# Kernel optimization log

Measured on AMD Instinct MI355X. Metric: run time of the kernel, lower is better.

Reference implementation:

```python
import jax, jax.numpy as jnp
import numpy as np

N_NODES = 100000
N_EDGES = 200000  # per relation
D_NODE = 128
D_EDGE = 16
N_REL = 3  # agent-agent, agent-object, object-object


def setup_inputs() -> dict:
    key = jax.random.key(0)
    ks = jax.random.split(key, 6)
    x = jax.random.normal(ks[0], (N_NODES, D_NODE), dtype=jnp.float32)
    edge_attr = jax.random.normal(ks[1], (N_REL, N_EDGES, D_EDGE), dtype=jnp.float32)
    W_rel = jax.random.normal(ks[2], (N_REL, D_NODE, D_NODE), dtype=jnp.float32) / np.sqrt(D_NODE)
    We_rel = jax.random.normal(ks[3], (N_REL, D_EDGE, D_NODE), dtype=jnp.float32) / np.sqrt(D_EDGE)
    W_self = jax.random.normal(ks[4], (D_NODE, D_NODE), dtype=jnp.float32) / np.sqrt(D_NODE)
    b = jnp.zeros((D_NODE,), dtype=jnp.float32)
    edge_index = jax.random.randint(ks[5], (N_REL, N_EDGES, 2), 0, N_NODES, dtype=jnp.int32)
    return {"x": x, "edge_attr": edge_attr, "W_rel": W_rel, "We_rel": We_rel,
            "W_self": W_self, "b": b, "edge_index": edge_index}


def reference(x, edge_attr, W_rel, We_rel, W_self, b, edge_index):
    # Heterogeneous message passing: per relation r,
    #   msg_e = x[src_e] @ W_r + edge_attr_e @ We_r
    #   agg_r = scatter_add(msg, dst)
    # node update: relu(x @ W_self + sum_r agg_r + b)
    n = x.shape[0]
    src = edge_index[:, :, 0]  # [R, E]
    dst = edge_index[:, :, 1]  # [R, E]
    # gather source features per relation: [R, E, F]
    msgs = jnp.einsum('ref,rfo->reo', x[src], W_rel) \
         + jnp.einsum('reg,rgo->reo', edge_attr, We_rel)
    # scatter-add to destination nodes per relation -> [R, N, F]
    agg = jax.vmap(lambda m, d: jax.ops.segment_sum(m, d, num_segments=n))(msgs, dst)
    return jax.nn.relu(x @ W_self + agg.sum(axis=0) + b)
```

## Files before the change

kernel.cpp:

```cpp
#include <hip/hip_runtime.h>

#define NN 100000
#define NE 200000
#define DN 128
#define DE 16
#define NR 3
#define NEDGE (NR * NE)
#define NB1 98
#define NSTRIP 6250
#define GEMM_GRID 1024

typedef __attribute__((ext_vector_type(8))) short short8;
typedef __attribute__((ext_vector_type(4))) float f32x4;

__device__ __forceinline__ unsigned short f2bf(float f) {
    unsigned int u = __float_as_uint(f);
    u = (u + 0x7fffu + ((u >> 16) & 1u)) >> 16;
    return (unsigned short)u;
}

__global__ __launch_bounds__(256) void prep_kernel(
    const float* __restrict__ W_self, const float* __restrict__ W_rel,
    const float* __restrict__ We,
    unsigned short* __restrict__ Wt, unsigned short* __restrict__ Wea,
    const int* __restrict__ ei, unsigned* __restrict__ cur,
    unsigned char* __restrict__ tmp)
{
    const int id = blockIdx.x * 256 + threadIdx.x;
    if (id < 65536) {
        const int m = id >> 14, rem = id & 16383;
        const int k = rem >> 7, n = rem & 127;
        const float* src = (m == 0) ? W_self : (W_rel + (size_t)(m - 1) * 16384);
        Wt[m * 16384 + n * 128 + k] = f2bf(src[k * 128 + n]);
    } else if (id < 65536 + 8192) {
        const int wid = id - 65536;
        const int n = wid >> 6, k = wid & 63;
        const float v = (k < 48) ? We[(k >> 4) * 2048 + (k & 15) * 128 + n] : 0.f;
        Wea[n * 64 + k] = f2bf(v);
    }
    const int2* ei2 = (const int2*)ei;
    for (int eid = id; eid < NEDGE; eid += 262144) {
        const int2 e = ei2[eid];
        const unsigned pos = atomicAdd(&cur[e.y], 1u);
        tmp[eid] = (unsigned char)pos;
    }
}

__global__ __launch_bounds__(256, 2) void gemm_kernel(
    const float* __restrict__ x,
    const unsigned short* __restrict__ Wt,
    unsigned short* __restrict__ zb,
    unsigned short* __restrict__ y)
{
    const int tid = threadIdx.x;
    const int m = tid >> 6;
    const int lane = tid & 63;
    const int lm = lane & 15;
    const int lq = lane >> 4;

    short8 bfr[8][4];
    {
        const unsigned short* wp = Wt + (size_t)m * 16384;
        #pragma unroll
        for (int cg = 0; cg < 8; ++cg)
            #pragma unroll
            for (int ks = 0; ks < 4; ++ks)
                bfr[cg][ks] = *(const short8*)(wp + (cg * 16 + lm) * 128 + ks * 32 + lq * 8);
    }
    unsigned short* outp = (m == 0) ? zb : (y + (size_t)(m - 1) * NN * 128);

    int s = blockIdx.x;
    float4 xb[8];
    {
        const float* xp = x + (size_t)(s * 16 + lm) * 128 + lq * 8;
        #pragma unroll
        for (int ks = 0; ks < 4; ++ks) {
            xb[2 * ks]     = *(const float4*)(xp + ks * 32);
            xb[2 * ks + 1] = *(const float4*)(xp + ks * 32 + 4);
        }
    }

    while (true) {
        short8 af[4];
        #pragma unroll
        for (int ks = 0; ks < 4; ++ks) {
            short8 t;
            t[0] = f2bf(xb[2 * ks].x);     t[1] = f2bf(xb[2 * ks].y);
            t[2] = f2bf(xb[2 * ks].z);     t[3] = f2bf(xb[2 * ks].w);
            t[4] = f2bf(xb[2 * ks + 1].x); t[5] = f2bf(xb[2 * ks + 1].y);
            t[6] = f2bf(xb[2 * ks + 1].z); t[7] = f2bf(xb[2 * ks + 1].w);
            af[ks] = t;
        }
        const int sn = s + GEMM_GRID;
        if (sn < NSTRIP) {
            const float* xp = x + (size_t)(sn * 16 + lm) * 128 + lq * 8;
            #pragma unroll
            for (int ks = 0; ks < 4; ++ks) {
                xb[2 * ks]     = *(const float4*)(xp + ks * 32);
                xb[2 * ks + 1] = *(const float4*)(xp + ks * 32 + 4);
            }
        }
        f32x4 acc[8];
        #pragma unroll
        for (int cg = 0; cg < 8; ++cg) acc[cg] = (f32x4){0.f, 0.f, 0.f, 0.f};
        #pragma unroll
        for (int cg = 0; cg < 8; ++cg)
            #pragma unroll
            for (int ks = 0; ks < 4; ++ks)
                acc[cg] = __builtin_amdgcn_mfma_f32_16x16x32_bf16(bfr[cg][ks], af[ks], acc[cg], 0, 0, 0);
        unsigned short* rp = outp + (size_t)(s * 16 + lm) * 128 + lq * 4;
        #pragma unroll
        for (int cg = 0; cg < 8; ++cg) {
            ushort4 o;
            o.x = f2bf(acc[cg][0]); o.y = f2bf(acc[cg][1]);
            o.z = f2bf(acc[cg][2]); o.w = f2bf(acc[cg][3]);
            *(ushort4*)(rp + cg * 16) = o;
        }
        if (sn >= NSTRIP) break;
        s = sn;
    }
}

__global__ __launch_bounds__(256) void scan1_kernel(
    const unsigned* __restrict__ cnt, unsigned* __restrict__ offs,
    unsigned* __restrict__ bsum)
{
    __shared__ unsigned wtot[4];
    const int tid = threadIdx.x, lane = tid & 63, wv = tid >> 6;
    const int base = blockIdx.x * 1024 + tid * 4;
    unsigned c[4];
    #pragma unroll
    for (int j = 0; j < 4; ++j) c[j] = (base + j < NN) ? cnt[base + j] : 0u;
    const unsigned ts = c[0] + c[1] + c[2] + c[3];
    unsigned incl = ts;
    #pragma unroll
    for (int d = 1; d < 64; d <<= 1) {
        unsigned v = __shfl_up(incl, d, 64);
        if (lane >= d) incl += v;
    }
    if (lane == 63) wtot[wv] = incl;
    __syncthreads();
    unsigned woff = 0;
    for (int p = 0; p < 4; ++p) if (p < wv) woff += wtot[p];
    unsigned run = woff + incl - ts;
    #pragma unroll
    for (int j = 0; j < 4; ++j) {
        if (base + j < NN) offs[base + j] = run;
        run += c[j];
    }
    if (tid == 255) bsum[blockIdx.x] = woff + incl;
}

__global__ void scan2_kernel(unsigned* __restrict__ bsum)
{
    const int lane = threadIdx.x;
    unsigned v[2], s = 0;
    const int base = lane * 2;
    #pragma unroll
    for (int j = 0; j < 2; ++j) {
        v[j] = (base + j < NB1) ? bsum[base + j] : 0u;
        s += v[j];
    }
    unsigned incl = s;
    #pragma unroll
    for (int d = 1; d < 64; d <<= 1) {
        unsigned t = __shfl_up(incl, d, 64);
        if (lane >= d) incl += t;
    }
    unsigned run = incl - s;
    #pragma unroll
    for (int j = 0; j < 2; ++j) {
        if (base + j < NB1) bsum[base + j] = run;
        run += v[j];
    }
}

__global__ __launch_bounds__(256) void scan3_kernel(
    unsigned* __restrict__ offs, const unsigned* __restrict__ bsum)
{
    const int base = blockIdx.x * 1024 + threadIdx.x * 4;
    const unsigned add = bsum[blockIdx.x];
    #pragma unroll
    for (int j = 0; j < 4; ++j)
        if (base + j < NN) offs[base + j] += add;
    if (blockIdx.x == 0 && threadIdx.x == 0) offs[NN] = NEDGE;
}

__global__ __launch_bounds__(256) void fill_kernel(
    const int* __restrict__ ei, const unsigned* __restrict__ offs,
    const unsigned char* __restrict__ tmp,
    unsigned* __restrict__ erow, unsigned* __restrict__ eeid)
{
    const int eid = blockIdx.x * 256 + threadIdx.x;
    if (eid < NEDGE) {
        const int2 e = ((const int2*)ei)[eid];
        const unsigned r = (eid >= 2 * NE) ? 2u : (eid >= NE ? 1u : 0u);
        const unsigned pos = offs[e.y] + (unsigned)tmp[eid];
        erow[pos] = r * NN + (unsigned)e.x;
        eeid[pos] = (unsigned)eid;
    }
}

__global__ __launch_bounds__(256, 4) void eaz_kernel(
    const float* __restrict__ edge_attr,
    const unsigned short* __restrict__ Wea,
    const unsigned* __restrict__ offs,
    const unsigned* __restrict__ eeid,
    unsigned short* __restrict__ zb)
{
    __shared__ __align__(16) unsigned short eaS[16][64];
    const int tid = threadIdx.x;
    const int wv = tid >> 6, lane = tid & 63;
    const int g = lane >> 4;
    const int k16 = lane & 15;
    const int row0 = blockIdx.x * 16;

    #pragma unroll
    for (int d = 0; d < 4; ++d) {
        const int dst = row0 + wv * 4 + d;
        const unsigned s = __builtin_amdgcn_readfirstlane(offs[dst]);
        const unsigned e = __builtin_amdgcn_readfirstlane(offs[dst + 1]);
        float ea = 0.f;
        unsigned py[8];
        #pragma unroll
        for (int j = 0; j < 8; ++j) {
            const unsigned q = eeid[s + j];
            py[j] = (q < (unsigned)NEDGE) ? q : 0u;
        }
        float a[8];
        #pragma unroll
        for (int j = 0; j < 8; ++j)
            a[j] = edge_attr[(size_t)py[j] * 16 + k16];
        #pragma unroll
        for (int j = 0; j < 8; ++j) {
            const bool ok = ((s + (unsigned)j) < e)
                && py[j] >= (unsigned)(g * NE) && py[j] < (unsigned)((g + 1) * NE);
            ea += ok ? a[j] : 0.f;
        }
        for (unsigned i = s + 8; i < e; ++i) {
            const unsigned q = eeid[i];
            const float av = edge_attr[(size_t)q * 16 + k16];
            const bool ok = q >= (unsigned)(g * NE) && q < (unsigned)((g + 1) * NE);
            ea += ok ? av : 0.f;
        }
        eaS[wv * 4 + d][lane] = f2bf(ea);
    }
    __syncthreads();

    const int lm = lane & 15, lq = lane >> 4;
    const short8 af0 = *(const short8*)&eaS[lm][lq * 8];
    const short8 af1 = *(const short8*)&eaS[lm][32 + lq * 8];
    #pragma unroll
    for (int h = 0; h < 2; ++h) {
        const int cg = wv * 2 + h;
        const short8 b0 = *(const short8*)(Wea + (cg * 16 + lm) * 64 + lq * 8);
        const short8 b1 = *(const short8*)(Wea + (cg * 16 + lm) * 64 + 32 + lq * 8);
        f32x4 acc = {0.f, 0.f, 0.f, 0.f};
        acc = __builtin_amdgcn_mfma_f32_16x16x32_bf16(b0, af0, acc, 0, 0, 0);
        acc = __builtin_amdgcn_mfma_f32_16x16x32_bf16(b1, af1, acc, 0, 0, 0);
        unsigned short* zp = zb + (size_t)(row0 + lm) * 128 + cg * 16 + lq * 4;
        const ushort4 old = *(const ushort4*)zp;
        ushort4 o;
        o.x = f2bf(__uint_as_float((unsigned)old.x << 16) + acc[0]);
        o.y = f2bf(__uint_as_float((unsigned)old.y << 16) + acc[1]);
        o.z = f2bf(__uint_as_float((unsigned)old.z << 16) + acc[2]);
        o.w = f2bf(__uint_as_float((unsigned)old.w << 16) + acc[3]);
        *(ushort4*)zp = o;
    }
}

__global__ __launch_bounds__(256, 4) void aggregate_kernel(
    const unsigned short* __restrict__ zb,
    const unsigned short* __restrict__ y,
    const float* __restrict__ b,
    const unsigned* __restrict__ offs,
    const unsigned* __restrict__ erow,
    float* __restrict__ out)
{
    const int tid = threadIdx.x;
    const int wv = tid >> 6, lane = tid & 63;
    const int dst0 = (blockIdx.x * 4 + wv) * 4;
    const int col = 2 * lane;

    unsigned sI[4], eI[4];
    #pragma unroll
    for (int d = 0; d < 4; ++d) {
        sI[d] = __builtin_amdgcn_readfirstlane(offs[dst0 + d]);
        eI[d] = __builtin_amdgcn_readfirstlane(offs[dst0 + d + 1]);
    }

    unsigned r[4][8];
    #pragma unroll
    for (int d = 0; d < 4; ++d) {
        #pragma unroll
        for (int j = 0; j < 8; ++j) {
            const unsigned q = erow[sI[d] + j];
            r[d][j] = (q < 3u * NN) ? q : 0u;
        }
    }

    unsigned v[4][8];
    #pragma unroll
    for (int d = 0; d < 4; ++d)
        #pragma unroll
        for (int j = 0; j < 8; ++j)
            v[d][j] = *(const unsigned*)(y + (size_t)r[d][j] * 128 + col);

    float acc0[4], acc1[4];
    #pragma unroll
    for (int d = 0; d < 4; ++d) {
        const unsigned zv = *(const unsigned*)(zb + (size_t)(dst0 + d) * 128 + col);
        acc0[d] = __uint_as_float(zv << 16);
        acc1[d] = __uint_as_float(zv & 0xffff0000u);
    }

    #pragma unroll
    for (int d = 0; d < 4; ++d)
        #pragma unroll
        for (int j = 0; j < 8; ++j) {
            const unsigned vv = ((sI[d] + (unsigned)j) < eI[d]) ? v[d][j] : 0u;
            acc0[d] += __uint_as_float(vv << 16);
            acc1[d] += __uint_as_float(vv & 0xffff0000u);
        }

    #pragma unroll
    for (int d = 0; d < 4; ++d)
        for (unsigned i = sI[d] + 8; i < eI[d]; ++i) {
            const unsigned vv = *(const unsigned*)(y + (size_t)erow[i] * 128 + col);
            acc0[d] += __uint_as_float(vv << 16);
            acc1[d] += __uint_as_float(vv & 0xffff0000u);
        }

    const float2 bv = *(const float2*)(b + col);
    #pragma unroll
    for (int d = 0; d < 4; ++d) {
        float2 o;
        o.x = fmaxf(acc0[d] + bv.x, 0.f);
        o.y = fmaxf(acc1[d] + bv.y, 0.f);
        *(float2*)(out + (size_t)(dst0 + d) * 128 + col) = o;
    }
}

extern "C" void kernel_launch(void* const* d_in, const int* in_sizes, int n_in,
                              void* d_out, int out_size, void* d_ws, size_t ws_size,
                              hipStream_t stream)
{
    const float* x         = (const float*)d_in[0];
    const float* edge_attr = (const float*)d_in[1];
    const float* W_rel     = (const float*)d_in[2];
    const float* We_rel    = (const float*)d_in[3];
    const float* W_self    = (const float*)d_in[4];
    const float* b         = (const float*)d_in[5];
    const int*   edge_index= (const int*)d_in[6];
    float* out = (float*)d_out;

    char* wsb = (char*)d_ws;
    unsigned short* zb   = (unsigned short*)wsb;
    unsigned short* y    = (unsigned short*)(wsb + 25600000);
    unsigned short* Wt   = (unsigned short*)(wsb + 102400000);
    unsigned short* Wea  = (unsigned short*)(wsb + 102531072);
    unsigned*       cur  = (unsigned*)(wsb + 102547456);
    unsigned*       offs = (unsigned*)(wsb + 102947456);
    unsigned*       bsum = (unsigned*)(wsb + 103347460);
    unsigned*       erow = (unsigned*)(wsb + 103347972);
    unsigned*       eeid = (unsigned*)(wsb + 105748004);
    unsigned char*  tmp  = (unsigned char*)(wsb + 108148036);

    hipMemsetAsync(cur, 0, NN * sizeof(unsigned), stream);
    prep_kernel<<<1024, 256, 0, stream>>>(W_self, W_rel, We_rel, Wt, Wea,
                                          edge_index, cur, tmp);
    gemm_kernel<<<GEMM_GRID, 256, 0, stream>>>(x, Wt, zb, y);

    scan1_kernel<<<NB1, 256, 0, stream>>>(cur, offs, bsum);
    scan2_kernel<<<1, 64, 0, stream>>>(bsum);
    scan3_kernel<<<NB1, 256, 0, stream>>>(offs, bsum);
    const int eblocks = (NEDGE + 255) / 256;
    fill_kernel <<<eblocks, 256, 0, stream>>>(edge_index, offs, tmp, erow, eeid);

    eaz_kernel<<<NN / 16, 256, 0, stream>>>(edge_attr, Wea, offs, eeid, zb);
    aggregate_kernel<<<NN / 16, 256, 0, stream>>>(zb, y, b, offs, erow, out);
}
```

Before: 317.8 us.

## Fuse edge-attr projection into aggregation, restructure GEMM with LDS weights, merge scans

Merges the eaz and aggregate kernels so each destination row gathers y messages and edge attributes in one pass. The edge-attr MFMA result is added to the row sums in LDS before relu, which removes the zb read-modify-write round trip and a kernel launch. Interleaves erow/eeid into a single uint2 edge list, and fuses scan2 into scan3. The GEMM now gives one weight matrix per block, held in swizzled LDS instead of registers, with 4096 blocks, which trades register pressure for LDS reads.

```diff
diff --git a/kernel.cpp b/kernel.cpp
--- a/kernel.cpp
+++ b/kernel.cpp
@@ -8,7 +8,6 @@
 #define NEDGE (NR * NE)
 #define NB1 98
 #define NSTRIP 6250
-#define GEMM_GRID 1024
 
 typedef __attribute__((ext_vector_type(8))) short short8;
 typedef __attribute__((ext_vector_type(4))) float f32x4;
@@ -31,7 +30,8 @@
         const int m = id >> 14, rem = id & 16383;
         const int k = rem >> 7, n = rem & 127;
         const float* src = (m == 0) ? W_self : (W_rel + (size_t)(m - 1) * 16384);
-        Wt[m * 16384 + n * 128 + k] = f2bf(src[k * 128 + n]);
+        Wt[m * 16384 + n * 128 + (((k >> 3) ^ (n & 7)) << 3) + (k & 7)] =
+            f2bf(src[k * 128 + n]);
     } else if (id < 65536 + 8192) {
         const int wid = id - 65536;
         const int n = wid >> 6, k = wid & 63;
@@ -46,30 +46,31 @@
     }
 }
 
-__global__ __launch_bounds__(256, 2) void gemm_kernel(
+__global__ __launch_bounds__(256, 3) void gemm_kernel(
     const float* __restrict__ x,
     const unsigned short* __restrict__ Wt,
     unsigned short* __restrict__ zb,
     unsigned short* __restrict__ y)
 {
+    __shared__ __align__(16) unsigned short Bs[128 * 128];
     const int tid = threadIdx.x;
-    const int m = tid >> 6;
+    const int m = blockIdx.x & 3;
+    const int sblk = blockIdx.x >> 2;
     const int lane = tid & 63;
     const int lm = lane & 15;
     const int lq = lane >> 4;
 
-    short8 bfr[8][4];
     {
-        const unsigned short* wp = Wt + (size_t)m * 16384;
-        #pragma unroll
-        for (int cg = 0; cg < 8; ++cg)
-            #pragma unroll
-            for (int ks = 0; ks < 4; ++ks)
-                bfr[cg][ks] = *(const short8*)(wp + (cg * 16 + lm) * 128 + ks * 32 + lq * 8);
-    }
+        const uint4* wp4 = (const uint4*)(Wt + (size_t)m * 16384);
+        #pragma unroll
+        for (int i = 0; i < 8; ++i)
+            *(uint4*)&Bs[(tid + i * 256) * 8] = wp4[tid + i * 256];
+    }
+    __syncthreads();
+
     unsigned short* outp = (m == 0) ? zb : (y + (size_t)(m - 1) * NN * 128);
 
-    int s = blockIdx.x;
+    int s = sblk;
     float4 xb[8];
     {
         const float* xp = x + (size_t)(s * 16 + lm) * 128 + lq * 8;
@@ -91,7 +92,7 @@
             t[6] = f2bf(xb[2 * ks + 1].z); t[7] = f2bf(xb[2 * ks + 1].w);
             af[ks] = t;
         }
-        const int sn = s + GEMM_GRID;
+        const int sn = s + 1024;
         if (sn < NSTRIP) {
             const float* xp = x + (size_t)(sn * 16 + lm) * 128 + lq * 8;
             #pragma unroll
@@ -106,8 +107,11 @@
         #pragma unroll
         for (int cg = 0; cg < 8; ++cg)
             #pragma unroll
-            for (int ks = 0; ks < 4; ++ks)
-                acc[cg] = __builtin_amdgcn_mfma_f32_16x16x32_bf16(bfr[cg][ks], af[ks], acc[cg], 0, 0, 0);
+            for (int ks = 0; ks < 4; ++ks) {
+                const short8 bf = *(const short8*)
+                    &Bs[(cg * 16 + lm) * 128 + (((ks * 4 + lq) ^ (lm & 7)) << 3)];
+                acc[cg] = __builtin_amdgcn_mfma_f32_16x16x32_bf16(bf, af[ks], acc[cg], 0, 0, 0);
+            }
         unsigned short* rp = outp + (size_t)(s * 16 + lm) * 128 + lq * 4;
         #pragma unroll
         for (int cg = 0; cg < 8; ++cg) {
@@ -151,99 +155,139 @@
     if (tid == 255) bsum[blockIdx.x] = woff + incl;
 }
 
-__global__ void scan2_kernel(unsigned* __restrict__ bsum)
-{
-    const int lane = threadIdx.x;
-    unsigned v[2], s = 0;
-    const int base = lane * 2;
-    #pragma unroll
-    for (int j = 0; j < 2; ++j) {
-        v[j] = (base + j < NB1) ? bsum[base + j] : 0u;
-        s += v[j];
-    }
-    unsigned incl = s;
-    #pragma unroll
-    for (int d = 1; d < 64; d <<= 1) {
-        unsigned t = __shfl_up(incl, d, 64);
-        if (lane >= d) incl += t;
-    }
-    unsigned run = incl - s;
-    #pragma unroll
-    for (int j = 0; j < 2; ++j) {
-        if (base + j < NB1) bsum[base + j] = run;
-        run += v[j];
-    }
-}
-
-__global__ __launch_bounds__(256) void scan3_kernel(
+__global__ __launch_bounds__(256) void scan23_kernel(
     unsigned* __restrict__ offs, const unsigned* __restrict__ bsum)
 {
-    const int base = blockIdx.x * 1024 + threadIdx.x * 4;
-    const unsigned add = bsum[blockIdx.x];
+    __shared__ unsigned add_s;
+    const int tid = threadIdx.x;
+    if (tid < 64) {
+        const int lane = tid;
+        const unsigned v0 = (2 * lane     < NB1) ? bsum[2 * lane]     : 0u;
+        const unsigned v1 = (2 * lane + 1 < NB1) ? bsum[2 * lane + 1] : 0u;
+        const unsigned s = v0 + v1;
+        unsigned incl = s;
+        #pragma unroll
+        for (int d = 1; d < 64; d <<= 1) {
+            unsigned t = __shfl_up(incl, d, 64);
+            if (lane >= d) incl += t;
+        }
+        const unsigned run = incl - s;
+        if (lane == (blockIdx.x >> 1))
+            add_s = (blockIdx.x & 1) ? (run + v0) : run;
+    }
+    __syncthreads();
+    const unsigned add = add_s;
+    const int base = blockIdx.x * 1024 + tid * 4;
     #pragma unroll
     for (int j = 0; j < 4; ++j)
         if (base + j < NN) offs[base + j] += add;
-    if (blockIdx.x == 0 && threadIdx.x == 0) offs[NN] = NEDGE;
+    if (blockIdx.x == 0 && tid == 0) offs[NN] = NEDGE;
 }
 
 __global__ __launch_bounds__(256) void fill_kernel(
     const int* __restrict__ ei, const unsigned* __restrict__ offs,
-    const unsigned char* __restrict__ tmp,
-    unsigned* __restrict__ erow, unsigned* __restrict__ eeid)
+    const unsigned char* __restrict__ tmp, uint2* __restrict__ elist)
 {
     const int eid = blockIdx.x * 256 + threadIdx.x;
     if (eid < NEDGE) {
         const int2 e = ((const int2*)ei)[eid];
         const unsigned r = (eid >= 2 * NE) ? 2u : (eid >= NE ? 1u : 0u);
         const unsigned pos = offs[e.y] + (unsigned)tmp[eid];
-        erow[pos] = r * NN + (unsigned)e.x;
-        eeid[pos] = (unsigned)eid;
-    }
-}
-
-__global__ __launch_bounds__(256, 4) void eaz_kernel(
+        elist[pos] = make_uint2(r * NN + (unsigned)e.x, (unsigned)eid);
+    }
+}
+
+__global__ __launch_bounds__(256, 4) void aggregate_kernel(
+    const unsigned short* __restrict__ zb,
+    const unsigned short* __restrict__ y,
     const float* __restrict__ edge_attr,
     const unsigned short* __restrict__ Wea,
+    const float* __restrict__ b,
     const unsigned* __restrict__ offs,
-    const unsigned* __restrict__ eeid,
-    unsigned short* __restrict__ zb)
-{
-    __shared__ __align__(16) unsigned short eaS[16][64];
+    const uint2* __restrict__ elist,
+    float* __restrict__ out)
+{
+    __shared__ __align__(16) unsigned short eaS[16][72];
+    __shared__ __align__(16) float ysumS[16][132];
     const int tid = threadIdx.x;
     const int wv = tid >> 6, lane = tid & 63;
+    const int row0 = blockIdx.x * 16;
+    const int dst0 = row0 + wv * 4;
+    const int col = 2 * lane;
+    const int k16 = lane & 15;
     const int g = lane >> 4;
-    const int k16 = lane & 15;
-    const int row0 = blockIdx.x * 16;
-
+
+    unsigned sI[4], eI[4];
     #pragma unroll
     for (int d = 0; d < 4; ++d) {
-        const int dst = row0 + wv * 4 + d;
-        const unsigned s = __builtin_amdgcn_readfirstlane(offs[dst]);
-        const unsigned e = __builtin_amdgcn_readfirstlane(offs[dst + 1]);
-        float ea = 0.f;
-        unsigned py[8];
+        sI[d] = __builtin_amdgcn_readfirstlane(offs[dst0 + d]);
+        eI[d] = __builtin_amdgcn_readfirstlane(offs[dst0 + d + 1]);
+    }
+
+    unsigned r[4][8], q[4][8];
+    #pragma unroll
+    for (int d = 0; d < 4; ++d) {
+        const uint2* ep = elist + sI[d];
         #pragma unroll
         for (int j = 0; j < 8; ++j) {
-            const unsigned q = eeid[s + j];
-            py[j] = (q < (unsigned)NEDGE) ? q : 0u;
-        }
-        float a[8];
+            const uint2 p = ep[j];
+            r[d][j] = (p.x < 3u * NN) ? p.x : 0u;
+            q[d][j] = (p.y < (unsigned)NEDGE) ? p.y : 0u;
+        }
+    }
+
+    unsigned v[4][8];
+    #pragma unroll
+    for (int d = 0; d < 4; ++d)
         #pragma unroll
         for (int j = 0; j < 8; ++j)
-            a[j] = edge_attr[(size_t)py[j] * 16 + k16];
+            v[d][j] = *(const unsigned*)(y + (size_t)r[d][j] * 128 + col);
+    float a[4][8];
+    #pragma unroll
+    for (int d = 0; d < 4; ++d)
+        #pragma unroll
+        for (int j = 0; j < 8; ++j)
+            a[d][j] = edge_attr[(size_t)q[d][j] * 16 + k16];
+
+    float acc0[4], acc1[4], ea[4];
+    #pragma unroll
+    for (int d = 0; d < 4; ++d) {
+        const unsigned zv = *(const unsigned*)(zb + (size_t)(dst0 + d) * 128 + col);
+        acc0[d] = __uint_as_float(zv << 16);
+        acc1[d] = __uint_as_float(zv & 0xffff0000u);
+        ea[d] = 0.f;
+    }
+
+    #pragma unroll
+    for (int d = 0; d < 4; ++d)
         #pragma unroll
         for (int j = 0; j < 8; ++j) {
-            const bool ok = ((s + (unsigned)j) < e)
-                && py[j] >= (unsigned)(g * NE) && py[j] < (unsigned)((g + 1) * NE);
-            ea += ok ? a[j] : 0.f;
-        }
-        for (unsigned i = s + 8; i < e; ++i) {
-            const unsigned q = eeid[i];
-            const float av = edge_attr[(size_t)q * 16 + k16];
-            const bool ok = q >= (unsigned)(g * NE) && q < (unsigned)((g + 1) * NE);
-            ea += ok ? av : 0.f;
-        }
-        eaS[wv * 4 + d][lane] = f2bf(ea);
+            const bool live = (sI[d] + (unsigned)j) < eI[d];
+            const unsigned vv = live ? v[d][j] : 0u;
+            acc0[d] += __uint_as_float(vv << 16);
+            acc1[d] += __uint_as_float(vv & 0xffff0000u);
+            const bool okr = live && q[d][j] >= (unsigned)(g * NE)
+                                  && q[d][j] < (unsigned)((g + 1) * NE);
+            ea[d] += okr ? a[d][j] : 0.f;
+        }
+
+    #pragma unroll
+    for (int d = 0; d < 4; ++d)
+        for (unsigned i = sI[d] + 8; i < eI[d]; ++i) {
+            const uint2 p = elist[i];
+            const unsigned vv = *(const unsigned*)(y + (size_t)p.x * 128 + col);
+            const float aa = edge_attr[(size_t)p.y * 16 + k16];
+            acc0[d] += __uint_as_float(vv << 16);
+            acc1[d] += __uint_as_float(vv & 0xffff0000u);
+            const bool okr = p.y >= (unsigned)(g * NE) && p.y < (unsigned)((g + 1) * NE);
+            ea[d] += okr ? aa : 0.f;
+        }
+
+    #pragma unroll
+    for (int d = 0; d < 4; ++d) {
+        eaS[wv * 4 + d][lane] = f2bf(ea[d]);
+        ysumS[wv * 4 + d][col] = acc0[d];
+        ysumS[wv * 4 + d][col + 1] = acc1[d];
     }
     __syncthreads();
 
@@ -258,86 +302,15 @@
         f32x4 acc = {0.f, 0.f, 0.f, 0.f};
         acc = __builtin_amdgcn_mfma_f32_16x16x32_bf16(b0, af0, acc, 0, 0, 0);
         acc = __builtin_amdgcn_mfma_f32_16x16x32_bf16(b1, af1, acc, 0, 0, 0);
-        unsigned short* zp = zb + (size_t)(row0 + lm) * 128 + cg * 16 + lq * 4;
-        const ushort4 old = *(const ushort4*)zp;
-        ushort4 o;
-        o.x = f2bf(__uint_as_float((unsigned)old.x << 16) + acc[0]);
-        o.y = f2bf(__uint_as_float((unsigned)old.y << 16) + acc[1]);
-        o.z = f2bf(__uint_as_float((unsigned)old.z << 16) + acc[2]);
-        o.w = f2bf(__uint_as_float((unsigned)old.w << 16) + acc[3]);
-        *(ushort4*)zp = o;
-    }
-}
-
-__global__ __launch_bounds__(256, 4) void aggregate_kernel(
-    const unsigned short* __restrict__ zb,
-    const unsigned short* __restrict__ y,
-    const float* __restrict__ b,
-    const unsigned* __restrict__ offs,
-    const unsigned* __restrict__ erow,
-    float* __restrict__ out)
-{
-    const int tid = threadIdx.x;
-    const int wv = tid >> 6, lane = tid & 63;
-    const int dst0 = (blockIdx.x * 4 + wv) * 4;
-    const int col = 2 * lane;
-
-    unsigned sI[4], eI[4];
-    #pragma unroll
-    for (int d = 0; d < 4; ++d) {
-        sI[d] = __builtin_amdgcn_readfirstlane(offs[dst0 + d]);
-        eI[d] = __builtin_amdgcn_readfirstlane(offs[dst0 + d + 1]);
-    }
-
-    unsigned r[4][8];
-    #pragma unroll
-    for (int d = 0; d < 4; ++d) {
-        #pragma unroll
-        for (int j = 0; j < 8; ++j) {
-            const unsigned q = erow[sI[d] + j];
-            r[d][j] = (q < 3u * NN) ? q : 0u;
-        }
-    }
-
-    unsigned v[4][8];
-    #pragma unroll
-    for (int d = 0; d < 4; ++d)
-        #pragma unroll
-        for (int j = 0; j < 8; ++j)
-            v[d][j] = *(const unsigned*)(y + (size_t)r[d][j] * 128 + col);
-
-    float acc0[4], acc1[4];
-    #pragma unroll
-    for (int d = 0; d < 4; ++d) {
-        const unsigned zv = *(const unsigned*)(zb + (size_t)(dst0 + d) * 128 + col);
-        acc0[d] = __uint_as_float(zv << 16);
-        acc1[d] = __uint_as_float(zv & 0xffff0000u);
-    }
-
-    #pragma unroll
-    for (int d = 0; d < 4; ++d)
-        #pragma unroll
-        for (int j = 0; j < 8; ++j) {
-            const unsigned vv = ((sI[d] + (unsigned)j) < eI[d]) ? v[d][j] : 0u;
-            acc0[d] += __uint_as_float(vv << 16);
-            acc1[d] += __uint_as_float(vv & 0xffff0000u);
-        }
-
-    #pragma unroll
-    for (int d = 0; d < 4; ++d)
-        for (unsigned i = sI[d] + 8; i < eI[d]; ++i) {
-            const unsigned vv = *(const unsigned*)(y + (size_t)erow[i] * 128 + col);
-            acc0[d] += __uint_as_float(vv << 16);
-            acc1[d] += __uint_as_float(vv & 0xffff0000u);
-        }
-
-    const float2 bv = *(const float2*)(b + col);
-    #pragma unroll
-    for (int d = 0; d < 4; ++d) {
-        float2 o;
-        o.x = fmaxf(acc0[d] + bv.x, 0.f);
-        o.y = fmaxf(acc1[d] + bv.y, 0.f);
-        *(float2*)(out + (size_t)(dst0 + d) * 128 + col) = o;
+        const int c0 = cg * 16 + lq * 4;
+        const float4 ys = *(const float4*)&ysumS[lm][c0];
+        const float4 bv = *(const float4*)(b + c0);
+        float4 o;
+        o.x = fmaxf(ys.x + acc[0] + bv.x, 0.f);
+        o.y = fmaxf(ys.y + acc[1] + bv.y, 0.f);
+        o.z = fmaxf(ys.z + acc[2] + bv.z, 0.f);
+        o.w = fmaxf(ys.w + acc[3] + bv.w, 0.f);
+        *(float4*)(out + (size_t)(row0 + lm) * 128 + c0) = o;
     }
 }
 
@@ -362,21 +335,19 @@
     unsigned*       cur  = (unsigned*)(wsb + 102547456);
     unsigned*       offs = (unsigned*)(wsb + 102947456);
     unsigned*       bsum = (unsigned*)(wsb + 103347460);
-    unsigned*       erow = (unsigned*)(wsb + 103347972);
-    unsigned*       eeid = (unsigned*)(wsb + 105748004);
-    unsigned char*  tmp  = (unsigned char*)(wsb + 108148036);
+    uint2*          elist= (uint2*)(wsb + 103347976);
+    unsigned char*  tmp  = (unsigned char*)(wsb + 108148040);
 
     hipMemsetAsync(cur, 0, NN * sizeof(unsigned), stream);
     prep_kernel<<<1024, 256, 0, stream>>>(W_self, W_rel, We_rel, Wt, Wea,
                                           edge_index, cur, tmp);
-    gemm_kernel<<<GEMM_GRID, 256, 0, stream>>>(x, Wt, zb, y);
+    gemm_kernel<<<4096, 256, 0, stream>>>(x, Wt, zb, y);
 
     scan1_kernel<<<NB1, 256, 0, stream>>>(cur, offs, bsum);
-    scan2_kernel<<<1, 64, 0, stream>>>(bsum);
-    scan3_kernel<<<NB1, 256, 0, stream>>>(offs, bsum);
+    scan23_kernel<<<NB1, 256, 0, stream>>>(offs, bsum);
     const int eblocks = (NEDGE + 255) / 256;
-    fill_kernel <<<eblocks, 256, 0, stream>>>(edge_index, offs, tmp, erow, eeid);
-
-    eaz_kernel<<<NN / 16, 256, 0, stream>>>(edge_attr, Wea, offs, eeid, zb);
-    aggregate_kernel<<<NN / 16, 256, 0, stream>>>(zb, y, b, offs, erow, out);
-}
+    fill_kernel <<<eblocks, 256, 0, stream>>>(edge_index, offs, tmp, elist);
+
+    aggregate_kernel<<<NN / 16, 256, 0, stream>>>(zb, y, edge_attr, Wea, b,
+                                                  offs, elist, out);
+}
```

Result: slower. 610.0 us (+92.0%).
